# Optimization experiments

Hardware: AMD Instinct MI355X
Metric: run time of the kernel (lower is better)

## Reference

```python
import jax, jax.numpy as jnp
import numpy as np

B, Z, A, D = 2048, 128, 4, 50000
EPS = 1e-8


def setup_inputs() -> dict:
    key = jax.random.key(0)
    k1, k2, k3, k4, k5 = jax.random.split(key, 5)
    return {
        "batch_x": jax.random.normal(k1, (B, Z), dtype=jnp.float32),
        "batch_next": jax.random.normal(k2, (B, Z), dtype=jnp.float32),
        "keys": jax.random.normal(k3, (A, D, Z), dtype=jnp.float32),
        "vals": jax.random.normal(k4, (A, D, Z), dtype=jnp.float32),
        "batch_a": jax.random.randint(k5, (B,), 0, A, dtype=jnp.int64),
    }


def _dnd_lookup(q, keys_a, vals_a):
    # q: [B, Z] (L2-normalized), keys_a: [D, Z], vals_a: [D, Z]
    kn = keys_a / (jnp.linalg.norm(keys_a, axis=-1, keepdims=True) + EPS)
    sims = jnp.einsum("bz,dz->bd", q, kn)          # cosine similarity [B, D]
    w = jax.nn.softmax(sims, axis=-1)                # attention over dictionary
    return jnp.einsum("bd,dz->bz", w, vals_a)       # [B, Z]


def reference(batch_x, batch_next, keys, vals, batch_a):
    # Per-sample routed DND lookup: each sample queries the memory of its action,
    # then MSE loss vs batch_next (eval-mode trainBatch; memory write is a state
    # mutation done after the loss and does not affect the returned value).
    qn = batch_x / (jnp.linalg.norm(batch_x, axis=-1, keepdims=True) + EPS)
    a_space = keys.shape[0]
    pred = jnp.zeros_like(batch_x)
    for a in range(a_space):  # small fixed loop over distinct memories
        pred_a = _dnd_lookup(qn, keys[a], vals[a])
        pred = jnp.where((batch_a == a)[:, None], pred_a, pred)
    return jnp.mean((pred - batch_next) ** 2)
```

## Files before the change

kernel.cpp:

```cpp
#include <hip/hip_runtime.h>
#include <stdint.h>

#define B_N 2048
#define Z_N 128
#define A_N 4
#define D_N 50000
#define D_PAD 51200
#define EPS_F 1e-8f

#define TILE_B 128
#define KT 32
#define NSPLIT 64
#define SPAN 800
#define NITER 25
#define KL_S 140
#define VL_S 40

typedef __attribute__((ext_vector_type(8))) short short8;
typedef __attribute__((ext_vector_type(4))) float f32x4;
typedef __attribute__((ext_vector_type(2))) unsigned int u32x2;

__device__ __forceinline__ unsigned short f2bf(float f) {
  unsigned int u = __builtin_bit_cast(unsigned int, f);
  u += 0x7FFFu + ((u >> 16) & 1u);
  return (unsigned short)(u >> 16);
}

__device__ __forceinline__ void plswap32(unsigned int& a, unsigned int& b) {
#if __has_builtin(__builtin_amdgcn_permlane32_swap)
  u32x2 r = __builtin_amdgcn_permlane32_swap(a, b, false, false);
  a = r[0]; b = r[1];
#else
  asm volatile("v_permlane32_swap_b32 %0, %1" : "+v"(a), "+v"(b));
#endif
}
__device__ __forceinline__ void plswap16(unsigned int& a, unsigned int& b) {
#if __has_builtin(__builtin_amdgcn_permlane16_swap)
  u32x2 r = __builtin_amdgcn_permlane16_swap(a, b, false, false);
  a = r[0]; b = r[1];
#else
  asm volatile("v_permlane16_swap_b32 %0, %1" : "+v"(a), "+v"(b));
#endif
}

__global__ void k_norm(const float* __restrict__ keys, const float* __restrict__ x,
                       unsigned short* __restrict__ kn, unsigned short* __restrict__ qnb) {
  int w = threadIdx.x >> 6, lane = threadIdx.x & 63;
  int row = blockIdx.x * 4 + w;
  const float* src;
  unsigned short* dst;
  if (row >= A_N * D_PAD) {
    int r = row - A_N * D_PAD;
    src = x + (size_t)r * Z_N;
    dst = qnb + (size_t)r * Z_N;
  } else {
    int a = row / D_PAD, d = row - a * D_PAD;
    dst = kn + (size_t)row * Z_N;
    if (d >= D_N) { ((unsigned int*)dst)[lane] = 0u; return; }
    src = keys + ((size_t)a * D_N + d) * Z_N;
  }
  const float2 v = ((const float2*)src)[lane];
  float ss = v.x * v.x + v.y * v.y;
#pragma unroll
  for (int m = 1; m < 64; m <<= 1) ss += __shfl_xor(ss, m);
  float inv = 1.0f / (sqrtf(ss) + EPS_F);
  unsigned int packed = ((unsigned int)f2bf(v.y * inv) << 16) | f2bf(v.x * inv);
  ((unsigned int*)dst)[lane] = packed;
}

__global__ void k_vtrans(const float* __restrict__ vals, unsigned short* __restrict__ vt) {
  __shared__ float tile[64][65];
  int a = blockIdx.z, d0 = blockIdx.x * 64, z0 = blockIdx.y * 64;
  int t = threadIdx.x;
  int r = t >> 4, c4 = (t & 15) * 4;
#pragma unroll
  for (int i = 0; i < 4; ++i) {
    int dr = r + i * 16, d = d0 + dr;
    float4 v = {0.f, 0.f, 0.f, 0.f};
    if (d < D_N) v = *(const float4*)(vals + ((size_t)a * D_N + d) * Z_N + z0 + c4);
    tile[dr][c4 + 0] = v.x; tile[dr][c4 + 1] = v.y;
    tile[dr][c4 + 2] = v.z; tile[dr][c4 + 3] = v.w;
  }
  __syncthreads();
  int zz = t >> 2, dg = (t & 3) * 16;
  union { unsigned short u[16]; uint4 q[2]; } pk;
#pragma unroll
  for (int j = 0; j < 16; ++j) pk.u[j] = f2bf(tile[dg + j][zz]);
  unsigned short* dst = vt + ((size_t)a * Z_N + z0 + zz) * D_PAD + d0 + dg;
  ((uint4*)dst)[0] = pk.q[0];
  ((uint4*)dst)[1] = pk.q[1];
}

__global__ void k_route(const int* __restrict__ act, int* __restrict__ counts,
                        int* __restrict__ lists, int* __restrict__ work) {
  __shared__ int lc[4];
  int t = threadIdx.x;
  if (t < 4) lc[t] = 0;
  __syncthreads();
  for (int i = t; i < B_N; i += 1024) {
    int a = act[i];
    int pos = atomicAdd(&lc[a], 1);
    lists[a * B_N + pos] = i;
  }
  __syncthreads();
  if (t < 4) counts[t] = lc[t];
  int t0 = (lc[0] + TILE_B - 1) >> 7, t1 = (lc[1] + TILE_B - 1) >> 7;
  int t2 = (lc[2] + TILE_B - 1) >> 7, t3 = (lc[3] + TILE_B - 1) >> 7;
  int T = t0 + t1 + t2 + t3;
  int total = T * NSPLIT;
  if (t == 0) work[0] = total;
  for (int i = t; i < total; i += 1024) {
    int lo = i & 7, q = i >> 3;
    int chi = q / T, j = q - chi * T;
    int c = (chi << 3) | lo;
    int a, ty;
    if (j < t0)                { a = 0; ty = j; }
    else if (j < t0 + t1)      { a = 1; ty = j - t0; }
    else if (j < t0 + t1 + t2) { a = 2; ty = j - t0 - t1; }
    else                       { a = 3; ty = j - t0 - t1 - t2; }
    work[1 + i] = a | (ty << 2) | (c << 8);
  }
}

__launch_bounds__(512)
__global__ void k_flash(const unsigned short* __restrict__ kn,
                        const unsigned short* __restrict__ vt,
                        const unsigned short* __restrict__ qnb,
                        const int* __restrict__ counts,
                        const int* __restrict__ lists,
                        const int* __restrict__ work,
                        float* __restrict__ acc,
                        float* __restrict__ sume) {
  int total = work[0];
  if ((int)blockIdx.x >= total) return;
  int wi = work[1 + blockIdx.x];
  int a = wi & 3, ty = (wi >> 2) & 63, span = wi >> 8;
  int nb = counts[a];

  __shared__ unsigned short Kl[2][KT * KL_S];
  __shared__ unsigned short Vl[2][128 * VL_S];

  int t = threadIdx.x;
  int w = t >> 6, lane = t & 63;
  int lq = lane >> 4, ln = lane & 15;

  const unsigned short* kn_a = kn + (size_t)a * D_PAD * Z_N;
  const unsigned short* vt_a = vt + (size_t)a * Z_N * D_PAD;
  const int* list_a = lists + a * B_N;

  int g0 = ty * TILE_B + w * 16 + ln;
  bool qvalid = g0 < nb;
  int si0 = qvalid ? list_a[g0] : 0;
  short8 qf[4];
#pragma unroll
  for (int c = 0; c < 4; ++c) {
    short8 s = (short8){0,0,0,0,0,0,0,0};
    if (qvalid) s = *(const short8*)(qnb + (size_t)si0 * Z_N + c * 32 + lq * 8);
    qf[c] = s;
  }

  f32x4 O[8];
#pragma unroll
  for (int zt = 0; zt < 8; ++zt) O[zt] = (f32x4){0.f, 0.f, 0.f, 0.f};
  float rs = 0.f;

  int d_base = span * SPAN;
  int sk_key = t >> 4, sk_z = (t & 15) * 8;
  int sv_z = t >> 2, sv_k = (t & 3) * 8;

  uint4 kp, vp;

#define LOAD_TILE(d)                                                          \
  {                                                                           \
    kp = *(const uint4*)(kn_a + (size_t)((d) + sk_key) * Z_N + sk_z);         \
    vp = *(const uint4*)(vt_a + (size_t)sv_z * D_PAD + (d) + sv_k);           \
  }
#define STORE_TILE(p)                                                         \
  {                                                                           \
    *(uint4*)&Kl[p][sk_key * KL_S + sk_z] = kp;                               \
    *(uint4*)&Vl[p][sv_z * VL_S + sv_k] = vp;                                 \
  }

  LOAD_TILE(d_base);
  STORE_TILE(0);
  LOAD_TILE(d_base + KT);
  __syncthreads();

  int p = 0;
  for (int kt = 0; kt < NITER; ++kt) {
    int d0 = d_base + kt * KT;
    if (kt + 1 < NITER) {
      STORE_TILE(p ^ 1);
      if (kt + 2 < NITER) LOAD_TILE(d0 + 2 * KT)
    }

    f32x4 ST[2];
#pragma unroll
    for (int nt = 0; nt < 2; ++nt) {
      short8 kf[4];
#pragma unroll
      for (int c = 0; c < 4; ++c)
        kf[c] = *(const short8*)&Kl[p][(nt * 16 + ln) * KL_S + c * 32 + lq * 8];
      f32x4 s4 = (f32x4){0.f, 0.f, 0.f, 0.f};
#pragma unroll
      for (int c = 0; c < 4; ++c)
        s4 = __builtin_amdgcn_mfma_f32_16x16x32_bf16(kf[c], qf[c], s4, 0, 0, 0);
      ST[nt] = s4;
    }

    unsigned int s00, s01, s10, s11;
#pragma unroll
    for (int nt = 0; nt < 2; ++nt) {
      float e0 = __expf(ST[nt][0]);
      float e1 = __expf(ST[nt][1]);
      float e2 = __expf(ST[nt][2]);
      float e3 = __expf(ST[nt][3]);
      rs += (e0 + e1) + (e2 + e3);
      unsigned int lo, hi;
      asm("v_cvt_pk_bf16_f32 %0, %1, %2" : "=v"(lo) : "v"(e0), "v"(e1));
      asm("v_cvt_pk_bf16_f32 %0, %1, %2" : "=v"(hi) : "v"(e2), "v"(e3));
      if (nt == 0) { s00 = lo; s01 = hi; } else { s10 = lo; s11 = hi; }
    }

    plswap32(s00, s10);
    plswap32(s01, s11);
    plswap16(s00, s10);
    plswap16(s01, s11);
    union { unsigned int u[4]; short8 v; } pa;
    pa.u[0] = s00; pa.u[1] = s01; pa.u[2] = s10; pa.u[3] = s11;

#pragma unroll
    for (int zt = 0; zt < 8; ++zt) {
      short8 vf = *(const short8*)&Vl[p][(zt * 16 + ln) * VL_S + lq * 8];
      O[zt] = __builtin_amdgcn_mfma_f32_16x16x32_bf16(pa.v, vf, O[zt], 0, 0, 0);
    }

    __syncthreads();
    p ^= 1;
  }

  rs += __shfl_xor(rs, 16);
  rs += __shfl_xor(rs, 32);

  if (lq == 0 && qvalid) atomicAdd(&sume[si0], rs);
#pragma unroll
  for (int r = 0; r < 4; ++r) {
    int g = ty * TILE_B + w * 16 + lq * 4 + r;
    if (g < nb) {
      int si = list_a[g];
      float* arow = acc + (size_t)si * Z_N + ln;
#pragma unroll
      for (int zt = 0; zt < 8; ++zt) atomicAdd(arow + zt * 16, O[zt][r]);
    }
  }
}

__global__ void k_loss(const float* __restrict__ acc, const float* __restrict__ sume,
                       const float* __restrict__ nxt, float* __restrict__ loss) {
  __shared__ float ls[4];
  int w = threadIdx.x >> 6, lane = threadIdx.x & 63;
  int row = blockIdx.x * 4 + w;
  float inv = 1.0f / (sume[row] - (float)(D_PAD - D_N));
  const float2 p2 = ((const float2*)(acc + (size_t)row * Z_N))[lane];
  const float2 n2 = ((const float2*)(nxt + (size_t)row * Z_N))[lane];
  float dx = p2.x * inv - n2.x, dy = p2.y * inv - n2.y;
  float s = dx * dx + dy * dy;
#pragma unroll
  for (int m = 1; m < 64; m <<= 1) s += __shfl_xor(s, m);
  if (lane == 0) ls[w] = s;
  __syncthreads();
  if (threadIdx.x == 0) atomicAdd(loss, ls[0] + ls[1] + ls[2] + ls[3]);
}

__global__ void k_final(const float* __restrict__ loss, float* __restrict__ out) {
  out[0] = loss[0] * (1.0f / (float)(B_N * Z_N));
}

extern "C" void kernel_launch(void* const* d_in, const int* in_sizes, int n_in,
                              void* d_out, int out_size, void* d_ws, size_t ws_size,
                              hipStream_t stream) {
  const float* x    = (const float*)d_in[0];
  const float* nxt  = (const float*)d_in[1];
  const float* keys = (const float*)d_in[2];
  const float* vals = (const float*)d_in[3];
  const int*   act  = (const int*)d_in[4];

  char* ws = (char*)d_ws;
  float* acc    = (float*)(ws + 0);
  float* sume   = (float*)(ws + 1048576);
  float* loss   = (float*)(ws + 1056768);
  int*   counts = (int*)(ws + 1056784);
  int*   lists  = (int*)(ws + 1056800);
  int*   work   = (int*)(ws + 1089568);
  unsigned short* qnb = (unsigned short*)(ws + 1097760);
  unsigned short* kn  = (unsigned short*)(ws + 1622048);
  unsigned short* vt  = (unsigned short*)(ws + 54050848);

  hipMemsetAsync(ws, 0, 1056784, stream);

  k_norm<<<51712, 256, 0, stream>>>(keys, x, kn, qnb);
  k_vtrans<<<dim3(800, 2, A_N), 256, 0, stream>>>(vals, vt);
  k_route<<<1, 1024, 0, stream>>>(act, counts, lists, work);
  k_flash<<<1216, 512, 0, stream>>>(kn, vt, qnb, counts, lists, work, acc, sume);
  k_loss<<<512, 256, 0, stream>>>(acc, sume, nxt, loss);
  k_final<<<1, 1, 0, stream>>>(loss, (float*)d_out);
}
```

Measured before the change: 385.0 us.

## Double query rows per flash tile and merge prep and final kernels

Each warp now processes two 16-row query groups (TILE_B 256), so every K/V tile staged in shared memory feeds twice as many MFMAs and the total K/V traffic through the flash kernel is halved. The grid shrinks from 1216 to 768 blocks. The norm and value-transpose kernels are merged into a single launch, and the final scaling is folded into the loss kernel's atomic, with the output zeroed by a memset. This removes launch overhead but raises register pressure from the doubled accumulators, and leaves fewer blocks to spread across the compute units.

```diff
diff --git a/kernel.cpp b/kernel.cpp
--- a/kernel.cpp
+++ b/kernel.cpp
@@ -8,13 +8,15 @@
 #define D_PAD 51200
 #define EPS_F 1e-8f
 
-#define TILE_B 128
+#define TILE_B 256
 #define KT 32
 #define NSPLIT 64
 #define SPAN 800
 #define NITER 25
 #define KL_S 140
 #define VL_S 40
+
+#define NORM_BLOCKS 51712
 
 typedef __attribute__((ext_vector_type(8))) short short8;
 typedef __attribute__((ext_vector_type(4))) float f32x4;
@@ -43,34 +45,39 @@
 #endif
 }
 
-__global__ void k_norm(const float* __restrict__ keys, const float* __restrict__ x,
-                       unsigned short* __restrict__ kn, unsigned short* __restrict__ qnb) {
-  int w = threadIdx.x >> 6, lane = threadIdx.x & 63;
-  int row = blockIdx.x * 4 + w;
-  const float* src;
-  unsigned short* dst;
-  if (row >= A_N * D_PAD) {
-    int r = row - A_N * D_PAD;
-    src = x + (size_t)r * Z_N;
-    dst = qnb + (size_t)r * Z_N;
-  } else {
-    int a = row / D_PAD, d = row - a * D_PAD;
-    dst = kn + (size_t)row * Z_N;
-    if (d >= D_N) { ((unsigned int*)dst)[lane] = 0u; return; }
-    src = keys + ((size_t)a * D_N + d) * Z_N;
-  }
-  const float2 v = ((const float2*)src)[lane];
-  float ss = v.x * v.x + v.y * v.y;
-#pragma unroll
-  for (int m = 1; m < 64; m <<= 1) ss += __shfl_xor(ss, m);
-  float inv = 1.0f / (sqrtf(ss) + EPS_F);
-  unsigned int packed = ((unsigned int)f2bf(v.y * inv) << 16) | f2bf(v.x * inv);
-  ((unsigned int*)dst)[lane] = packed;
-}
-
-__global__ void k_vtrans(const float* __restrict__ vals, unsigned short* __restrict__ vt) {
+__global__ void k_prep(const float* __restrict__ keys, const float* __restrict__ x,
+                       const float* __restrict__ vals,
+                       unsigned short* __restrict__ kn, unsigned short* __restrict__ qnb,
+                       unsigned short* __restrict__ vt) {
+  if (blockIdx.x < NORM_BLOCKS) {
+    int w = threadIdx.x >> 6, lane = threadIdx.x & 63;
+    int row = blockIdx.x * 4 + w;
+    const float* src;
+    unsigned short* dst;
+    if (row >= A_N * D_PAD) {
+      int r = row - A_N * D_PAD;
+      src = x + (size_t)r * Z_N;
+      dst = qnb + (size_t)r * Z_N;
+    } else {
+      int a = row / D_PAD, d = row - a * D_PAD;
+      dst = kn + (size_t)row * Z_N;
+      if (d >= D_N) { ((unsigned int*)dst)[lane] = 0u; return; }
+      src = keys + ((size_t)a * D_N + d) * Z_N;
+    }
+    const float2 v = ((const float2*)src)[lane];
+    float ss = v.x * v.x + v.y * v.y;
+#pragma unroll
+    for (int m = 1; m < 64; m <<= 1) ss += __shfl_xor(ss, m);
+    float inv = 1.0f / (sqrtf(ss) + EPS_F);
+    unsigned int packed = ((unsigned int)f2bf(v.y * inv) << 16) | f2bf(v.x * inv);
+    ((unsigned int*)dst)[lane] = packed;
+    return;
+  }
   __shared__ float tile[64][65];
-  int a = blockIdx.z, d0 = blockIdx.x * 64, z0 = blockIdx.y * 64;
+  int b = blockIdx.x - NORM_BLOCKS;
+  int bx = b % 800, rest = b / 800;
+  int by = rest & 1, a = rest >> 1;
+  int d0 = bx * 64, z0 = by * 64;
   int t = threadIdx.x;
   int r = t >> 4, c4 = (t & 15) * 4;
 #pragma unroll
@@ -104,8 +111,8 @@
   }
   __syncthreads();
   if (t < 4) counts[t] = lc[t];
-  int t0 = (lc[0] + TILE_B - 1) >> 7, t1 = (lc[1] + TILE_B - 1) >> 7;
-  int t2 = (lc[2] + TILE_B - 1) >> 7, t3 = (lc[3] + TILE_B - 1) >> 7;
+  int t0 = (lc[0] + TILE_B - 1) >> 8, t1 = (lc[1] + TILE_B - 1) >> 8;
+  int t2 = (lc[2] + TILE_B - 1) >> 8, t3 = (lc[3] + TILE_B - 1) >> 8;
   int T = t0 + t1 + t2 + t3;
   int total = T * NSPLIT;
   if (t == 0) work[0] = total;
@@ -148,21 +155,27 @@
   const unsigned short* vt_a = vt + (size_t)a * Z_N * D_PAD;
   const int* list_a = lists + a * B_N;
 
-  int g0 = ty * TILE_B + w * 16 + ln;
-  bool qvalid = g0 < nb;
-  int si0 = qvalid ? list_a[g0] : 0;
-  short8 qf[4];
-#pragma unroll
-  for (int c = 0; c < 4; ++c) {
-    short8 s = (short8){0,0,0,0,0,0,0,0};
-    if (qvalid) s = *(const short8*)(qnb + (size_t)si0 * Z_N + c * 32 + lq * 8);
-    qf[c] = s;
-  }
-
-  f32x4 O[8];
-#pragma unroll
-  for (int zt = 0; zt < 8; ++zt) O[zt] = (f32x4){0.f, 0.f, 0.f, 0.f};
-  float rs = 0.f;
+  short8 qf[2][4];
+  int si0[2]; bool qv[2];
+#pragma unroll
+  for (int m = 0; m < 2; ++m) {
+    int g0 = ty * TILE_B + w * 32 + m * 16 + ln;
+    qv[m] = g0 < nb;
+    si0[m] = qv[m] ? list_a[g0] : 0;
+#pragma unroll
+    for (int c = 0; c < 4; ++c) {
+      short8 s = (short8){0,0,0,0,0,0,0,0};
+      if (qv[m]) s = *(const short8*)(qnb + (size_t)si0[m] * Z_N + c * 32 + lq * 8);
+      qf[m][c] = s;
+    }
+  }
+
+  f32x4 O[2][8];
+#pragma unroll
+  for (int m = 0; m < 2; ++m)
+#pragma unroll
+    for (int zt = 0; zt < 8; ++zt) O[m][zt] = (f32x4){0.f, 0.f, 0.f, 0.f};
+  float rs[2] = {0.f, 0.f};
 
   int d_base = span * SPAN;
   int sk_key = t >> 4, sk_z = (t & 15) * 8;
@@ -194,69 +207,73 @@
       if (kt + 2 < NITER) LOAD_TILE(d0 + 2 * KT)
     }
 
-    f32x4 ST[2];
+    f32x4 ST[2][2];
 #pragma unroll
     for (int nt = 0; nt < 2; ++nt) {
-      short8 kf[4];
-#pragma unroll
-      for (int c = 0; c < 4; ++c)
-        kf[c] = *(const short8*)&Kl[p][(nt * 16 + ln) * KL_S + c * 32 + lq * 8];
-      f32x4 s4 = (f32x4){0.f, 0.f, 0.f, 0.f};
-#pragma unroll
-      for (int c = 0; c < 4; ++c)
-        s4 = __builtin_amdgcn_mfma_f32_16x16x32_bf16(kf[c], qf[c], s4, 0, 0, 0);
-      ST[nt] = s4;
-    }
-
-    unsigned int s00, s01, s10, s11;
-#pragma unroll
-    for (int nt = 0; nt < 2; ++nt) {
-      float e0 = __expf(ST[nt][0]);
-      float e1 = __expf(ST[nt][1]);
-      float e2 = __expf(ST[nt][2]);
-      float e3 = __expf(ST[nt][3]);
-      rs += (e0 + e1) + (e2 + e3);
-      unsigned int lo, hi;
-      asm("v_cvt_pk_bf16_f32 %0, %1, %2" : "=v"(lo) : "v"(e0), "v"(e1));
-      asm("v_cvt_pk_bf16_f32 %0, %1, %2" : "=v"(hi) : "v"(e2), "v"(e3));
-      if (nt == 0) { s00 = lo; s01 = hi; } else { s10 = lo; s11 = hi; }
-    }
-
-    plswap32(s00, s10);
-    plswap32(s01, s11);
-    plswap16(s00, s10);
-    plswap16(s01, s11);
-    union { unsigned int u[4]; short8 v; } pa;
-    pa.u[0] = s00; pa.u[1] = s01; pa.u[2] = s10; pa.u[3] = s11;
+      ST[nt][0] = (f32x4){0.f, 0.f, 0.f, 0.f};
+      ST[nt][1] = (f32x4){0.f, 0.f, 0.f, 0.f};
+#pragma unroll
+      for (int c = 0; c < 4; ++c) {
+        short8 kf = *(const short8*)&Kl[p][(nt * 16 + ln) * KL_S + c * 32 + lq * 8];
+        ST[nt][0] = __builtin_amdgcn_mfma_f32_16x16x32_bf16(kf, qf[0][c], ST[nt][0], 0, 0, 0);
+        ST[nt][1] = __builtin_amdgcn_mfma_f32_16x16x32_bf16(kf, qf[1][c], ST[nt][1], 0, 0, 0);
+      }
+    }
+
+    short8 pa[2];
+#pragma unroll
+    for (int m = 0; m < 2; ++m) {
+      float e0 = __expf(ST[0][m][0]), e1 = __expf(ST[0][m][1]);
+      float e2 = __expf(ST[0][m][2]), e3 = __expf(ST[0][m][3]);
+      float f0 = __expf(ST[1][m][0]), f1 = __expf(ST[1][m][1]);
+      float f2 = __expf(ST[1][m][2]), f3 = __expf(ST[1][m][3]);
+      rs[m] += ((e0 + e1) + (e2 + e3)) + ((f0 + f1) + (f2 + f3));
+      unsigned int s00, s01, s10, s11;
+      asm("v_cvt_pk_bf16_f32 %0, %1, %2" : "=v"(s00) : "v"(e0), "v"(e1));
+      asm("v_cvt_pk_bf16_f32 %0, %1, %2" : "=v"(s01) : "v"(e2), "v"(e3));
+      asm("v_cvt_pk_bf16_f32 %0, %1, %2" : "=v"(s10) : "v"(f0), "v"(f1));
+      asm("v_cvt_pk_bf16_f32 %0, %1, %2" : "=v"(s11) : "v"(f2), "v"(f3));
+      plswap32(s00, s10);
+      plswap32(s01, s11);
+      plswap16(s00, s10);
+      plswap16(s01, s11);
+      union { unsigned int u[4]; short8 v; } pk;
+      pk.u[0] = s00; pk.u[1] = s01; pk.u[2] = s10; pk.u[3] = s11;
+      pa[m] = pk.v;
+    }
 
 #pragma unroll
     for (int zt = 0; zt < 8; ++zt) {
       short8 vf = *(const short8*)&Vl[p][(zt * 16 + ln) * VL_S + lq * 8];
-      O[zt] = __builtin_amdgcn_mfma_f32_16x16x32_bf16(pa.v, vf, O[zt], 0, 0, 0);
+      O[0][zt] = __builtin_amdgcn_mfma_f32_16x16x32_bf16(pa[0], vf, O[0][zt], 0, 0, 0);
+      O[1][zt] = __builtin_amdgcn_mfma_f32_16x16x32_bf16(pa[1], vf, O[1][zt], 0, 0, 0);
     }
 
     __syncthreads();
     p ^= 1;
   }
 
-  rs += __shfl_xor(rs, 16);
-  rs += __shfl_xor(rs, 32);
-
-  if (lq == 0 && qvalid) atomicAdd(&sume[si0], rs);
-#pragma unroll
-  for (int r = 0; r < 4; ++r) {
-    int g = ty * TILE_B + w * 16 + lq * 4 + r;
-    if (g < nb) {
-      int si = list_a[g];
-      float* arow = acc + (size_t)si * Z_N + ln;
-#pragma unroll
-      for (int zt = 0; zt < 8; ++zt) atomicAdd(arow + zt * 16, O[zt][r]);
+#pragma unroll
+  for (int m = 0; m < 2; ++m) {
+    float r2 = rs[m];
+    r2 += __shfl_xor(r2, 16);
+    r2 += __shfl_xor(r2, 32);
+    if (lq == 0 && qv[m]) atomicAdd(&sume[si0[m]], r2);
+#pragma unroll
+    for (int r = 0; r < 4; ++r) {
+      int g = ty * TILE_B + w * 32 + m * 16 + lq * 4 + r;
+      if (g < nb) {
+        int si = list_a[g];
+        float* arow = acc + (size_t)si * Z_N + ln;
+#pragma unroll
+        for (int zt = 0; zt < 8; ++zt) atomicAdd(arow + zt * 16, O[m][zt][r]);
+      }
     }
   }
 }
 
 __global__ void k_loss(const float* __restrict__ acc, const float* __restrict__ sume,
-                       const float* __restrict__ nxt, float* __restrict__ loss) {
+                       const float* __restrict__ nxt, float* __restrict__ out) {
   __shared__ float ls[4];
   int w = threadIdx.x >> 6, lane = threadIdx.x & 63;
   int row = blockIdx.x * 4 + w;
@@ -269,11 +286,8 @@
   for (int m = 1; m < 64; m <<= 1) s += __shfl_xor(s, m);
   if (lane == 0) ls[w] = s;
   __syncthreads();
-  if (threadIdx.x == 0) atomicAdd(loss, ls[0] + ls[1] + ls[2] + ls[3]);
-}
-
-__global__ void k_final(const float* __restrict__ loss, float* __restrict__ out) {
-  out[0] = loss[0] * (1.0f / (float)(B_N * Z_N));
+  if (threadIdx.x == 0)
+    atomicAdd(out, (ls[0] + ls[1] + ls[2] + ls[3]) * (1.0f / (float)(B_N * Z_N)));
 }
 
 extern "C" void kernel_launch(void* const* d_in, const int* in_sizes, int n_in,
@@ -288,7 +302,6 @@
   char* ws = (char*)d_ws;
   float* acc    = (float*)(ws + 0);
   float* sume   = (float*)(ws + 1048576);
-  float* loss   = (float*)(ws + 1056768);
   int*   counts = (int*)(ws + 1056784);
   int*   lists  = (int*)(ws + 1056800);
   int*   work   = (int*)(ws + 1089568);
@@ -297,11 +310,10 @@
   unsigned short* vt  = (unsigned short*)(ws + 54050848);
 
   hipMemsetAsync(ws, 0, 1056784, stream);
-
-  k_norm<<<51712, 256, 0, stream>>>(keys, x, kn, qnb);
-  k_vtrans<<<dim3(800, 2, A_N), 256, 0, stream>>>(vals, vt);
+  hipMemsetAsync(d_out, 0, 4, stream);
+
   k_route<<<1, 1024, 0, stream>>>(act, counts, lists, work);
-  k_flash<<<1216, 512, 0, stream>>>(kn, vt, qnb, counts, lists, work, acc, sume);
-  k_loss<<<512, 256, 0, stream>>>(acc, sume, nxt, loss);
-  k_final<<<1, 1, 0, stream>>>(loss, (float*)d_out);
-}
+  k_prep<<<NORM_BLOCKS + 6400, 256, 0, stream>>>(keys, x, vals, kn, qnb, vt);
+  k_flash<<<768, 512, 0, stream>>>(kn, vt, qnb, counts, lists, work, acc, sume);
+  k_loss<<<512, 256, 0, stream>>>(acc, sume, nxt, (float*)d_out);
+}
```

New measurement: 395.5 us. 1.03x slower.

## Read key fragments directly from global memory, double KT, fuse prep and final kernels

Applied to the files above, without the earlier changes.

The flash kernel stops staging keys in LDS and has each lane load its MFMA key fragments straight from global memory, so only V is double-buffered in shared memory. The K tile grows to 64 with an inner two-step loop, which halves the barrier count, and the padding, span, iteration count and grid are changed to match. The norm and V-transpose kernels are merged into one launch, and the final scaling kernel is removed by having k_loss atomically add scaled partial sums into the output after a memset. The cost is uncoalesced direct global loads of K, which depend on cache hits, plus extra padded rows to process.

```diff
diff --git a/kernel.cpp b/kernel.cpp
--- a/kernel.cpp
+++ b/kernel.cpp
@@ -5,16 +5,18 @@
 #define Z_N 128
 #define A_N 4
 #define D_N 50000
-#define D_PAD 51200
+#define D_PAD 53248
 #define EPS_F 1e-8f
 
 #define TILE_B 128
-#define KT 32
+#define KT 64
 #define NSPLIT 64
-#define SPAN 800
-#define NITER 25
-#define KL_S 140
-#define VL_S 40
+#define SPAN 832
+#define NITER 13
+#define VL_S 72
+
+#define NORM_BLOCKS 53760
+#define VT_BX 832
 
 typedef __attribute__((ext_vector_type(8))) short short8;
 typedef __attribute__((ext_vector_type(4))) float f32x4;
@@ -43,34 +45,39 @@
 #endif
 }
 
-__global__ void k_norm(const float* __restrict__ keys, const float* __restrict__ x,
-                       unsigned short* __restrict__ kn, unsigned short* __restrict__ qnb) {
-  int w = threadIdx.x >> 6, lane = threadIdx.x & 63;
-  int row = blockIdx.x * 4 + w;
-  const float* src;
-  unsigned short* dst;
-  if (row >= A_N * D_PAD) {
-    int r = row - A_N * D_PAD;
-    src = x + (size_t)r * Z_N;
-    dst = qnb + (size_t)r * Z_N;
-  } else {
-    int a = row / D_PAD, d = row - a * D_PAD;
-    dst = kn + (size_t)row * Z_N;
-    if (d >= D_N) { ((unsigned int*)dst)[lane] = 0u; return; }
-    src = keys + ((size_t)a * D_N + d) * Z_N;
-  }
-  const float2 v = ((const float2*)src)[lane];
-  float ss = v.x * v.x + v.y * v.y;
-#pragma unroll
-  for (int m = 1; m < 64; m <<= 1) ss += __shfl_xor(ss, m);
-  float inv = 1.0f / (sqrtf(ss) + EPS_F);
-  unsigned int packed = ((unsigned int)f2bf(v.y * inv) << 16) | f2bf(v.x * inv);
-  ((unsigned int*)dst)[lane] = packed;
-}
-
-__global__ void k_vtrans(const float* __restrict__ vals, unsigned short* __restrict__ vt) {
+__global__ void k_prep(const float* __restrict__ keys, const float* __restrict__ x,
+                       const float* __restrict__ vals,
+                       unsigned short* __restrict__ kn, unsigned short* __restrict__ qnb,
+                       unsigned short* __restrict__ vt) {
+  if (blockIdx.x < NORM_BLOCKS) {
+    int w = threadIdx.x >> 6, lane = threadIdx.x & 63;
+    int row = blockIdx.x * 4 + w;
+    const float* src;
+    unsigned short* dst;
+    if (row >= A_N * D_PAD) {
+      int r = row - A_N * D_PAD;
+      src = x + (size_t)r * Z_N;
+      dst = qnb + (size_t)r * Z_N;
+    } else {
+      int a = row / D_PAD, d = row - a * D_PAD;
+      dst = kn + (size_t)row * Z_N;
+      if (d >= D_N) { ((unsigned int*)dst)[lane] = 0u; return; }
+      src = keys + ((size_t)a * D_N + d) * Z_N;
+    }
+    const float2 v = ((const float2*)src)[lane];
+    float ss = v.x * v.x + v.y * v.y;
+#pragma unroll
+    for (int m = 1; m < 64; m <<= 1) ss += __shfl_xor(ss, m);
+    float inv = 1.0f / (sqrtf(ss) + EPS_F);
+    unsigned int packed = ((unsigned int)f2bf(v.y * inv) << 16) | f2bf(v.x * inv);
+    ((unsigned int*)dst)[lane] = packed;
+    return;
+  }
   __shared__ float tile[64][65];
-  int a = blockIdx.z, d0 = blockIdx.x * 64, z0 = blockIdx.y * 64;
+  int b = blockIdx.x - NORM_BLOCKS;
+  int bx = b % VT_BX, rest = b / VT_BX;
+  int by = rest & 1, a = rest >> 1;
+  int d0 = bx * 64, z0 = by * 64;
   int t = threadIdx.x;
   int r = t >> 4, c4 = (t & 15) * 4;
 #pragma unroll
@@ -137,7 +144,6 @@
   int a = wi & 3, ty = (wi >> 2) & 63, span = wi >> 8;
   int nb = counts[a];
 
-  __shared__ unsigned short Kl[2][KT * KL_S];
   __shared__ unsigned short Vl[2][128 * VL_S];
 
   int t = threadIdx.x;
@@ -165,74 +171,77 @@
   float rs = 0.f;
 
   int d_base = span * SPAN;
-  int sk_key = t >> 4, sk_z = (t & 15) * 8;
-  int sv_z = t >> 2, sv_k = (t & 3) * 8;
-
-  uint4 kp, vp;
-
-#define LOAD_TILE(d)                                                          \
+
+  const unsigned short* kK = kn_a + (size_t)ln * Z_N + lq * 8;
+
+  int sr0 = t >> 3, sk0 = (t & 7) * 8;
+
+  uint4 vp0, vp1;
+
+#define LOADV(d)                                                              \
   {                                                                           \
-    kp = *(const uint4*)(kn_a + (size_t)((d) + sk_key) * Z_N + sk_z);         \
-    vp = *(const uint4*)(vt_a + (size_t)sv_z * D_PAD + (d) + sv_k);           \
-  }
-#define STORE_TILE(p)                                                         \
+    vp0 = *(const uint4*)(vt_a + (size_t)sr0 * D_PAD + (d) + sk0);            \
+    vp1 = *(const uint4*)(vt_a + (size_t)(sr0 + 64) * D_PAD + (d) + sk0);     \
+  }
+#define STOREV(p)                                                             \
   {                                                                           \
-    *(uint4*)&Kl[p][sk_key * KL_S + sk_z] = kp;                               \
-    *(uint4*)&Vl[p][sv_z * VL_S + sv_k] = vp;                                 \
-  }
-
-  LOAD_TILE(d_base);
-  STORE_TILE(0);
-  LOAD_TILE(d_base + KT);
+    *(uint4*)&Vl[p][sr0 * VL_S + sk0] = vp0;                                  \
+    *(uint4*)&Vl[p][(sr0 + 64) * VL_S + sk0] = vp1;                           \
+  }
+
+  LOADV(d_base);
+  STOREV(0);
+  LOADV(d_base + KT);
   __syncthreads();
 
   int p = 0;
   for (int kt = 0; kt < NITER; ++kt) {
     int d0 = d_base + kt * KT;
     if (kt + 1 < NITER) {
-      STORE_TILE(p ^ 1);
-      if (kt + 2 < NITER) LOAD_TILE(d0 + 2 * KT)
+      STOREV(p ^ 1);
+      if (kt + 2 < NITER) LOADV(d0 + 2 * KT)
     }
 
-    f32x4 ST[2];
-#pragma unroll
-    for (int nt = 0; nt < 2; ++nt) {
-      short8 kf[4];
-#pragma unroll
-      for (int c = 0; c < 4; ++c)
-        kf[c] = *(const short8*)&Kl[p][(nt * 16 + ln) * KL_S + c * 32 + lq * 8];
-      f32x4 s4 = (f32x4){0.f, 0.f, 0.f, 0.f};
-#pragma unroll
-      for (int c = 0; c < 4; ++c)
-        s4 = __builtin_amdgcn_mfma_f32_16x16x32_bf16(kf[c], qf[c], s4, 0, 0, 0);
-      ST[nt] = s4;
-    }
-
-    unsigned int s00, s01, s10, s11;
-#pragma unroll
-    for (int nt = 0; nt < 2; ++nt) {
-      float e0 = __expf(ST[nt][0]);
-      float e1 = __expf(ST[nt][1]);
-      float e2 = __expf(ST[nt][2]);
-      float e3 = __expf(ST[nt][3]);
-      rs += (e0 + e1) + (e2 + e3);
-      unsigned int lo, hi;
-      asm("v_cvt_pk_bf16_f32 %0, %1, %2" : "=v"(lo) : "v"(e0), "v"(e1));
-      asm("v_cvt_pk_bf16_f32 %0, %1, %2" : "=v"(hi) : "v"(e2), "v"(e3));
-      if (nt == 0) { s00 = lo; s01 = hi; } else { s10 = lo; s11 = hi; }
-    }
-
-    plswap32(s00, s10);
-    plswap32(s01, s11);
-    plswap16(s00, s10);
-    plswap16(s01, s11);
-    union { unsigned int u[4]; short8 v; } pa;
-    pa.u[0] = s00; pa.u[1] = s01; pa.u[2] = s10; pa.u[3] = s11;
-
-#pragma unroll
-    for (int zt = 0; zt < 8; ++zt) {
-      short8 vf = *(const short8*)&Vl[p][(zt * 16 + ln) * VL_S + lq * 8];
-      O[zt] = __builtin_amdgcn_mfma_f32_16x16x32_bf16(pa.v, vf, O[zt], 0, 0, 0);
+#pragma unroll
+    for (int kk = 0; kk < 2; ++kk) {
+      int dk = d0 + kk * 32;
+
+      f32x4 ST[2];
+#pragma unroll
+      for (int nt = 0; nt < 2; ++nt) {
+        const unsigned short* kb = kK + (size_t)(dk + nt * 16) * Z_N;
+        f32x4 s4 = (f32x4){0.f, 0.f, 0.f, 0.f};
+#pragma unroll
+        for (int c = 0; c < 4; ++c) {
+          short8 kf = *(const short8*)(kb + c * 32);
+          s4 = __builtin_amdgcn_mfma_f32_16x16x32_bf16(kf, qf[c], s4, 0, 0, 0);
+        }
+        ST[nt] = s4;
+      }
+
+      float e0 = __expf(ST[0][0]), e1 = __expf(ST[0][1]);
+      float e2 = __expf(ST[0][2]), e3 = __expf(ST[0][3]);
+      float f0 = __expf(ST[1][0]), f1 = __expf(ST[1][1]);
+      float f2 = __expf(ST[1][2]), f3 = __expf(ST[1][3]);
+      rs += ((e0 + e1) + (e2 + e3)) + ((f0 + f1) + (f2 + f3));
+      unsigned int s00, s01, s10, s11;
+      asm("v_cvt_pk_bf16_f32 %0, %1, %2" : "=v"(s00) : "v"(e0), "v"(e1));
+      asm("v_cvt_pk_bf16_f32 %0, %1, %2" : "=v"(s01) : "v"(e2), "v"(e3));
+      asm("v_cvt_pk_bf16_f32 %0, %1, %2" : "=v"(s10) : "v"(f0), "v"(f1));
+      asm("v_cvt_pk_bf16_f32 %0, %1, %2" : "=v"(s11) : "v"(f2), "v"(f3));
+
+      plswap32(s00, s10);
+      plswap32(s01, s11);
+      plswap16(s00, s10);
+      plswap16(s01, s11);
+      union { unsigned int u[4]; short8 v; } pa;
+      pa.u[0] = s00; pa.u[1] = s01; pa.u[2] = s10; pa.u[3] = s11;
+
+#pragma unroll
+      for (int zt = 0; zt < 8; ++zt) {
+        short8 vf = *(const short8*)&Vl[p][(zt * 16 + ln) * VL_S + kk * 32 + lq * 8];
+        O[zt] = __builtin_amdgcn_mfma_f32_16x16x32_bf16(pa.v, vf, O[zt], 0, 0, 0);
+      }
     }
 
     __syncthreads();
@@ -256,7 +265,7 @@
 }
 
 __global__ void k_loss(const float* __restrict__ acc, const float* __restrict__ sume,
-                       const float* __restrict__ nxt, float* __restrict__ loss) {
+                       const float* __restrict__ nxt, float* __restrict__ out) {
   __shared__ float ls[4];
   int w = threadIdx.x >> 6, lane = threadIdx.x & 63;
   int row = blockIdx.x * 4 + w;
@@ -269,11 +278,8 @@
   for (int m = 1; m < 64; m <<= 1) s += __shfl_xor(s, m);
   if (lane == 0) ls[w] = s;
   __syncthreads();
-  if (threadIdx.x == 0) atomicAdd(loss, ls[0] + ls[1] + ls[2] + ls[3]);
-}
-
-__global__ void k_final(const float* __restrict__ loss, float* __restrict__ out) {
-  out[0] = loss[0] * (1.0f / (float)(B_N * Z_N));
+  if (threadIdx.x == 0)
+    atomicAdd(out, (ls[0] + ls[1] + ls[2] + ls[3]) * (1.0f / (float)(B_N * Z_N)));
 }
 
 extern "C" void kernel_launch(void* const* d_in, const int* in_sizes, int n_in,
@@ -288,20 +294,18 @@
   char* ws = (char*)d_ws;
   float* acc    = (float*)(ws + 0);
   float* sume   = (float*)(ws + 1048576);
-  float* loss   = (float*)(ws + 1056768);
   int*   counts = (int*)(ws + 1056784);
   int*   lists  = (int*)(ws + 1056800);
   int*   work   = (int*)(ws + 1089568);
   unsigned short* qnb = (unsigned short*)(ws + 1097760);
   unsigned short* kn  = (unsigned short*)(ws + 1622048);
-  unsigned short* vt  = (unsigned short*)(ws + 54050848);
+  unsigned short* vt  = (unsigned short*)(ws + 56148000);
 
   hipMemsetAsync(ws, 0, 1056784, stream);
-
-  k_norm<<<51712, 256, 0, stream>>>(keys, x, kn, qnb);
-  k_vtrans<<<dim3(800, 2, A_N), 256, 0, stream>>>(vals, vt);
+  hipMemsetAsync(d_out, 0, 4, stream);
+
   k_route<<<1, 1024, 0, stream>>>(act, counts, lists, work);
-  k_flash<<<1216, 512, 0, stream>>>(kn, vt, qnb, counts, lists, work, acc, sume);
-  k_loss<<<512, 256, 0, stream>>>(acc, sume, nxt, loss);
-  k_final<<<1, 1, 0, stream>>>(loss, (float*)d_out);
-}
+  k_prep<<<NORM_BLOCKS + VT_BX * 2 * A_N, 256, 0, stream>>>(keys, x, vals, kn, qnb, vt);
+  k_flash<<<1280, 512, 0, stream>>>(kn, vt, qnb, counts, lists, work, acc, sume);
+  k_loss<<<512, 256, 0, stream>>>(acc, sume, nxt, (float*)d_out);
+}
```

New measurement: 579.9 us. +50.6%, slower.
